# Optimization experiments

Hardware: AMD Instinct MI355X
Metric: run time of the kernel (lower is better)

## Reference

```python
import jax, jax.numpy as jnp
import numpy as np

K, D = 2048, 256
B, H, W = 16, 64, 64
DECAY = 0.99
EPS = 1e-05


def setup_inputs() -> dict:
    key = jax.random.key(0)
    k1, k2, k3 = jax.random.split(key, 3)
    z_e = jax.random.normal(k1, (B, D, H, W), dtype=jnp.float32)
    codebook = jax.random.normal(k2, (K, D), dtype=jnp.float32)
    ema_count = jnp.zeros((K,), dtype=jnp.float32)
    ema_weight = jax.random.normal(k3, (K, D), dtype=jnp.float32)
    return {"z_e": z_e, "codebook": codebook, "ema_count": ema_count, "ema_weight": ema_weight}


def reference(z_e, codebook, ema_count, ema_weight):
    b, d, h, w = z_e.shape
    k = codebook.shape[0]
    # [B, D, H, W] -> [B*H*W, D]
    flat = jnp.transpose(z_e, (0, 2, 3, 1)).reshape(-1, d)
    # squared euclidean distances to each code: [N, K]
    dist = (jnp.sum(flat * flat, axis=1, keepdims=True)
            - 2.0 * (flat @ codebook.T)
            + jnp.sum(codebook * codebook, axis=1))
    idx = jnp.argmin(dist, axis=1)  # [N] int
    # gather nearest codes -> [B, D, H, W]
    z_q = jnp.transpose(codebook[idx].reshape(b, h, w, d), (0, 3, 1, 2))
    # EMA statistics (training path, no_grad in torch)
    n = jax.ops.segment_sum(jnp.ones_like(idx, dtype=flat.dtype), idx, num_segments=k)  # [K]
    dw = jax.ops.segment_sum(flat, idx, num_segments=k)  # [K, D]
    new_ema_count = ema_count * DECAY + (1.0 - DECAY) * n
    new_ema_weight = ema_weight * DECAY + (1.0 - DECAY) * dw
    new_codebook = new_ema_weight / (new_ema_count + EPS)[:, None]
    # commitment loss and straight-through estimator
    loss_commit = jnp.mean(jnp.square(z_e - z_q))
    z_q_st = z_e + jax.lax.stop_gradient(z_q - z_e)
    return (z_q_st, idx.reshape(b, h, w), loss_commit,
            new_codebook, new_ema_count, new_ema_weight)
```

## Files before the change

### kernel.cpp

```cpp
#include <hip/hip_runtime.h>
#include <hip/hip_bf16.h>


#define KC 2048
#define DD 256
#define NB 16
#define HWS 4096
#define NPTS 65536
#define DECAYF 0.99f
#define ONEMD 0.01f
#define EPSF 1e-5f
#define NCH 2
#define MARGIN 0.0625f
#define CHPTS 32
#define FPT 64
#define NLOSS 4096

typedef __attribute__((ext_vector_type(8))) short short8v;
typedef __attribute__((ext_vector_type(16))) float f32x16;

#define WS_IDX     0
#define WS_SORTED  262144
#define WS_CNTI    524288
#define WS_START   532480
#define WS_CURSOR  540672
#define WS_FLAGCNT 548864
#define WS_FLAGS   549120
#define WS_LOSSP   549120
#define WS_CNORM   811264
#define WS_PART    819456
#define WS_CBH     5013760
#define WS_CBL     6062336
#define WS_ZH      7110912
#define WS_ZL      40665344
#define WS_NEED_MFMA 74219776ULL
#define WS_NEED_MID  5013760ULL

#define OUT_ZQ   0
#define OUT_IDX  16777216
#define OUT_LOSS (OUT_IDX + NPTS)
#define OUT_CB   (OUT_LOSS + 1)
#define OUT_CNT  (OUT_CB + KC*DD)
#define OUT_W    (OUT_CNT + KC)

static __device__ __forceinline__ unsigned short f2bf_rn(float x) {
    unsigned u = __builtin_bit_cast(unsigned, x);
    unsigned r = (u + 0x7FFFu + ((u >> 16) & 1u)) >> 16;
    return (unsigned short)r;
}
static __device__ __forceinline__ float bf2f(unsigned short h) {
    unsigned u = ((unsigned)h) << 16;
    return __builtin_bit_cast(float, u);
}
static __device__ __forceinline__ void gload_lds16(const unsigned short* g,
                                                   unsigned short* l) {
    __builtin_amdgcn_global_load_lds(
        (const __attribute__((address_space(1))) void*)g,
        (__attribute__((address_space(3))) void*)l, 16, 0, 0);
}

__global__ __launch_bounds__(256) void prep_kernel(const float* __restrict__ z_e,
                                                   const float* __restrict__ cb,
                                                   float* __restrict__ cnorm,
                                                   unsigned short* __restrict__ cbs_h,
                                                   unsigned short* __restrict__ cbs_l,
                                                   unsigned short* __restrict__ zh,
                                                   unsigned short* __restrict__ zl,
                                                   int* __restrict__ cnti,
                                                   int* __restrict__ flagcnt) {
    const int tid = threadIdx.x;
    if (blockIdx.x >= 4096) {
        int k = (blockIdx.x - 4096) * 256 + tid;
        cnti[k] = 0;
        if (k == 0) *flagcnt = 0;
        const int ct = k >> 5, lc = k & 31;
        const float4* row = reinterpret_cast<const float4*>(cb + (size_t)k * DD);
        float s = 0.f;
        #pragma unroll 4
        for (int chunk = 0; chunk < 32; ++chunk) {
            float4 v0 = row[chunk * 2], v1 = row[chunk * 2 + 1];
            float v[8] = {v0.x, v0.y, v0.z, v0.w, v1.x, v1.y, v1.z, v1.w};
            unsigned short hh[8], ll[8];
            #pragma unroll
            for (int j = 0; j < 8; ++j) {
                s += v[j] * v[j];
                hh[j] = f2bf_rn(v[j]);
                ll[j] = f2bf_rn(v[j] - bf2f(hh[j]));
            }
            const int ks = chunk >> 1, h = chunk & 1;
            size_t dst = (size_t)ct * 8192 + ks * 512 + (h * 32 + lc) * 8;
            *reinterpret_cast<ushort4*>(cbs_h + dst)     = *(ushort4*)&hh[0];
            *reinterpret_cast<ushort4*>(cbs_h + dst + 4) = *(ushort4*)&hh[4];
            *reinterpret_cast<ushort4*>(cbs_l + dst)     = *(ushort4*)&ll[0];
            *reinterpret_cast<ushort4*>(cbs_l + dst + 4) = *(ushort4*)&ll[4];
        }
        cnorm[k] = s;
        return;
    }
    __shared__ float t_lds[64][65];
    const int bid = blockIdx.x;
    const int hw0 = (bid & 63) * 64;
    const int d0 = ((bid >> 6) & 3) * 64;
    const int b = bid >> 8;
    const float* src = z_e + (size_t)b * DD * HWS;
    #pragma unroll
    for (int i = 0; i < 16; ++i) {
        int li = tid + i * 256;
        int d = li >> 6, hw = li & 63;
        t_lds[d][hw] = src[(size_t)(d0 + d) * HWS + hw0 + hw];
    }
    __syncthreads();
    #pragma unroll
    for (int i = 0; i < 16; ++i) {
        int li = tid + i * 256;
        int p = li >> 6, d = li & 63;
        float x = t_lds[d][p];
        unsigned short h = f2bf_rn(x);
        unsigned short l = f2bf_rn(x - bf2f(h));
        size_t o = ((size_t)b * HWS + hw0 + p) * DD + d0 + d;
        zh[o] = h; zl[o] = l;
    }
}

__global__ __launch_bounds__(256) void cnorm_kernel(const float* __restrict__ cb,
                                                    float* __restrict__ cnorm) {
    int k = blockIdx.x * 256 + threadIdx.x;
    if (k < KC) {
        const float4* row = reinterpret_cast<const float4*>(cb + (size_t)k * DD);
        float s = 0.f;
        #pragma unroll 8
        for (int i = 0; i < DD / 4; ++i) {
            float4 v = row[i];
            s += v.x * v.x + v.y * v.y + v.z * v.z + v.w * v.w;
        }
        cnorm[k] = s;
    }
}

__global__ __launch_bounds__(256, 2) void argmin_mfma_kernel(const unsigned short* __restrict__ zh,
                                                             const unsigned short* __restrict__ zl,
                                                             const unsigned short* __restrict__ cbs_h,
                                                             const unsigned short* __restrict__ cbs_l,
                                                             const float* __restrict__ cnorm,
                                                             int* __restrict__ idx_out,
                                                             int* __restrict__ cnti,
                                                             int* __restrict__ flagcnt,
                                                             int* __restrict__ flaglist,
                                                             unsigned long long* __restrict__ fixmin) {
    __shared__ unsigned short lds_cb[2][16][512];

    const int tid = threadIdx.x;
    const int w = tid >> 6, lane = tid & 63;
    const int lc = lane & 31, h = lane >> 5;
    const int p = blockIdx.x * 128 + w * 32 + lc;

    const short8v* zhp = reinterpret_cast<const short8v*>(zh + (size_t)p * DD + h * 8);
    const short8v* zlp = reinterpret_cast<const short8v*>(zl + (size_t)p * DD + h * 8);
    short8v bh[16], bl[16];
    #pragma unroll
    for (int ks = 0; ks < 16; ++ks) { bh[ks] = zhp[ks * 2]; bl[ks] = zlp[ks * 2]; }

    auto stage = [&](int ct) {
        #pragma unroll
        for (int j = 0; j < 8; ++j) {
            const int inst = w * 8 + j;
            const int part = inst >> 4;
            const int ks = inst & 15;
            const unsigned short* src =
                (part ? cbs_l : cbs_h) + (size_t)ct * 8192 + ks * 512 + lane * 8;
            gload_lds16(src, &lds_cb[part][ks][0]);
        }
    };

    float bv1 = 3.4e38f, bv2 = 3.4e38f;
    int bi1 = 0;

    stage(0);
    __syncthreads();

    for (int ct = 0; ct < KC / 32; ++ct) {
        f32x16 a0, a1, a2;
        #pragma unroll
        for (int i = 0; i < 16; ++i) { a0[i] = 0.f; a1[i] = 0.f; a2[i] = 0.f; }
        #pragma unroll
        for (int ks = 0; ks < 16; ++ks) {
            short8v ah = *reinterpret_cast<const short8v*>(&lds_cb[0][ks][lane * 8]);
            short8v al = *reinterpret_cast<const short8v*>(&lds_cb[1][ks][lane * 8]);
            a0 = __builtin_amdgcn_mfma_f32_32x32x16_bf16(ah, bh[ks], a0, 0, 0, 0);
            a1 = __builtin_amdgcn_mfma_f32_32x32x16_bf16(ah, bl[ks], a1, 0, 0, 0);
            a2 = __builtin_amdgcn_mfma_f32_32x32x16_bf16(al, bh[ks], a2, 0, 0, 0);
        }
        const float* cnb = cnorm + ct * 32 + h * 4;
        #pragma unroll
        for (int g = 0; g < 4; ++g) {
            float4 cn = *reinterpret_cast<const float4*>(cnb + g * 8);
            float cna[4] = {cn.x, cn.y, cn.z, cn.w};
            #pragma unroll
            for (int q = 0; q < 4; ++q) {
                float dot = a0[g * 4 + q] + a1[g * 4 + q] + a2[g * 4 + q];
                float v = fmaf(dot, -2.0f, cna[q]);
                int k = ct * 32 + g * 8 + h * 4 + q;
                bool lt = v < bv1;
                bv2 = fminf(bv2, fmaxf(v, bv1));
                bv1 = fminf(bv1, v);
                bi1 = lt ? k : bi1;
            }
        }
        __syncthreads();
        if (ct + 1 < KC / 32) {
            stage(ct + 1);
            __syncthreads();
        }
    }

    float ov1 = __shfl_xor(bv1, 32, 64);
    float ov2 = __shfl_xor(bv2, 32, 64);
    int   oi1 = __shfl_xor(bi1, 32, 64);
    float nv1 = fminf(bv1, ov1);
    float nv2 = fminf(fmaxf(bv1, ov1), fminf(bv2, ov2));
    int ni1 = (ov1 < bv1 || (ov1 == bv1 && oi1 < bi1)) ? oi1 : bi1;

    if (h == 0) {
        idx_out[p] = ni1;
        atomicAdd(&cnti[ni1], 1);
        if (nv2 - nv1 < MARGIN) {
            int pos = atomicAdd(flagcnt, 1);
            flaglist[pos] = p;
            fixmin[pos] = ~0ULL;
        }
    }
}

__global__ __launch_bounds__(256) void fixup_part_kernel(const float* __restrict__ z_e,
                                                         const float* __restrict__ cb,
                                                         const float* __restrict__ cnorm,
                                                         const int* __restrict__ flagcnt,
                                                         const int* __restrict__ flaglist,
                                                         unsigned long long* __restrict__ fixmin) {
    __shared__ float As[64][FPT + 4];
    __shared__ float Bs[64][64 + 4];
    __shared__ float rv[FPT][16];
    __shared__ int   ri[FPT][16];
    __shared__ int   zo[FPT];

    const int tid = threadIdx.x;
    const int tx = tid & 15, ty = tid >> 4;
    const int tot = *flagcnt;
    const int kt = blockIdx.y * 64;

    for (int cbk = blockIdx.x; cbk * FPT < tot; cbk += gridDim.x) {
        const int base = cbk * FPT;
        const int cnt = min(FPT, tot - base);
        __syncthreads();
        if (tid < FPT) {
            int n = flaglist[base + ((tid < cnt) ? tid : 0)];
            zo[tid] = (n >> 12) * DD * HWS + (n & 4095);
        }
        __syncthreads();

        float acc[4][4] = {};
        for (int dc = 0; dc < DD; dc += 64) {
            #pragma unroll
            for (int i = 0; i < 16; ++i) {
                int li = tid + i * 256;
                int d = li >> 6, pp = li & 63;
                As[d][pp] = z_e[(size_t)zo[pp] + (size_t)(dc + d) * HWS];
            }
            #pragma unroll
            for (int i = 0; i < 16; ++i) {
                int li = tid + i * 256;
                int k = li >> 6, d = li & 63;
                Bs[d][k] = cb[(size_t)(kt + k) * DD + dc + d];
            }
            __syncthreads();
            #pragma unroll
            for (int d = 0; d < 64; ++d) {
                const float4 a4 = *reinterpret_cast<const float4*>(&As[d][ty * 4]);
                const float4 b4 = *reinterpret_cast<const float4*>(&Bs[d][tx * 4]);
                const float a[4] = {a4.x, a4.y, a4.z, a4.w};
                const float bb[4] = {b4.x, b4.y, b4.z, b4.w};
                #pragma unroll
                for (int j = 0; j < 4; ++j)
                    #pragma unroll
                    for (int i = 0; i < 4; ++i)
                        acc[j][i] = fmaf(a[j], bb[i], acc[j][i]);
            }
            __syncthreads();
        }

        float bestv[4]; int besti[4];
        #pragma unroll
        for (int j = 0; j < 4; ++j) { bestv[j] = 3.4e38f; besti[j] = 0; }
        #pragma unroll
        for (int i = 0; i < 4; ++i) {
            int k = kt + tx * 4 + i;
            float c = cnorm[k];
            #pragma unroll
            for (int j = 0; j < 4; ++j) {
                float dist = c - 2.0f * acc[j][i];
                if (dist < bestv[j]) { bestv[j] = dist; besti[j] = k; }
            }
        }
        #pragma unroll
        for (int j = 0; j < 4; ++j) { rv[ty * 4 + j][tx] = bestv[j]; ri[ty * 4 + j][tx] = besti[j]; }
        __syncthreads();

        if (tid < cnt) {
            float bv = rv[tid][0]; int bi = ri[tid][0];
            #pragma unroll
            for (int t = 1; t < 16; ++t) {
                float v = rv[tid][t]; int i2 = ri[tid][t];
                if (v < bv || (v == bv && i2 < bi)) { bv = v; bi = i2; }
            }
            unsigned uv = __float_as_uint(bv);
            uv = (uv & 0x80000000u) ? ~uv : (uv | 0x80000000u);
            unsigned long long key = ((unsigned long long)uv << 32) | (unsigned)bi;
            atomicMin(&fixmin[base + tid], key);
        }
    }
}

__global__ __launch_bounds__(256) void scan_apply_kernel(const int* __restrict__ flagcnt,
                                                         const int* __restrict__ flaglist,
                                                         const unsigned long long* __restrict__ fixmin,
                                                         int* __restrict__ idx_out,
                                                         int* __restrict__ cnti,
                                                         int* __restrict__ start,
                                                         int* __restrict__ cursor) {
    const int t = threadIdx.x;
    const int tot = *flagcnt;
    for (int f = t; f < tot; f += 256) {
        int n = flaglist[f];
        int nk = (int)(fixmin[f] & 0xFFFFFFFFull);
        int ok = idx_out[n];
        if (nk != ok) {
            atomicSub(&cnti[ok], 1);
            atomicAdd(&cnti[nk], 1);
            idx_out[n] = nk;
        }
    }
    __syncthreads();

    __shared__ int ps[256];
    int v[8], s = 0;
    #pragma unroll
    for (int j = 0; j < 8; ++j) { v[j] = cnti[t * 8 + j]; s += v[j]; }
    ps[t] = s;
    __syncthreads();
    for (int off = 1; off < 256; off <<= 1) {
        int x = (t >= off) ? ps[t - off] : 0;
        __syncthreads();
        ps[t] += x;
        __syncthreads();
    }
    int base = ps[t] - s;
    #pragma unroll
    for (int j = 0; j < 8; ++j) { start[t * 8 + j] = base; cursor[t * 8 + j] = base; base += v[j]; }
}

#define PT 64
#define KT 64
#define DC 64
__global__ __launch_bounds__(256) void argmin_kernel(const float* __restrict__ z_e,
                                                     const float* __restrict__ cb,
                                                     const float* __restrict__ cnorm,
                                                     int* __restrict__ idx_out) {
    __shared__ float As[DC][PT + 4];
    __shared__ float Bs[DC][KT + 4];
    __shared__ float rv[PT][16];
    __shared__ int   ri[PT][16];
    const int tid = threadIdx.x;
    const int tx = tid & 15, ty = tid >> 4;
    const int n0 = blockIdx.x * PT;
    const int b = n0 >> 12;
    const int hw0 = n0 & 4095;
    const float* zb = z_e + (size_t)b * DD * HWS + hw0;
    float bestv[4]; int besti[4];
    #pragma unroll
    for (int j = 0; j < 4; ++j) { bestv[j] = 3.4e38f; besti[j] = 0; }
    for (int kt = 0; kt < KC; kt += KT) {
        float acc[4][4] = {};
        for (int dc = 0; dc < DD; dc += DC) {
            #pragma unroll
            for (int i = 0; i < 16; ++i) {
                int li = tid + i * 256;
                int d = li >> 6, pp = li & 63;
                As[d][pp] = zb[(size_t)(dc + d) * HWS + pp];
            }
            #pragma unroll
            for (int i = 0; i < 16; ++i) {
                int li = tid + i * 256;
                int k = li >> 6, d = li & 63;
                Bs[d][k] = cb[(size_t)(kt + k) * DD + dc + d];
            }
            __syncthreads();
            #pragma unroll
            for (int d = 0; d < DC; ++d) {
                const float4 a4 = *reinterpret_cast<const float4*>(&As[d][ty * 4]);
                const float4 b4 = *reinterpret_cast<const float4*>(&Bs[d][tx * 4]);
                const float a[4] = {a4.x, a4.y, a4.z, a4.w};
                const float bb[4] = {b4.x, b4.y, b4.z, b4.w};
                #pragma unroll
                for (int j = 0; j < 4; ++j)
                    #pragma unroll
                    for (int i = 0; i < 4; ++i)
                        acc[j][i] = fmaf(a[j], bb[i], acc[j][i]);
            }
            __syncthreads();
        }
        #pragma unroll
        for (int i = 0; i < 4; ++i) {
            int k = kt + tx * 4 + i;
            float c = cnorm[k];
            #pragma unroll
            for (int j = 0; j < 4; ++j) {
                float dist = c - 2.0f * acc[j][i];
                if (dist < bestv[j]) { bestv[j] = dist; besti[j] = k; }
            }
        }
    }
    #pragma unroll
    for (int j = 0; j < 4; ++j) { rv[ty * 4 + j][tx] = bestv[j]; ri[ty * 4 + j][tx] = besti[j]; }
    __syncthreads();
    if (tid < PT) {
        float bv = rv[tid][0]; int bi = ri[tid][0];
        #pragma unroll
        for (int t = 1; t < 16; ++t) {
            float v = rv[tid][t]; int i2 = ri[tid][t];
            if (v < bv || (v == bv && i2 < bi)) { bv = v; bi = i2; }
        }
        idx_out[n0 + tid] = bi;
    }
}

__global__ __launch_bounds__(256) void hist_kernel(const int* __restrict__ idx,
                                                   int* __restrict__ cnti) {
    int n = blockIdx.x * 256 + threadIdx.x;
    atomicAdd(&cnti[idx[n]], 1);
}

__global__ __launch_bounds__(256) void scatter_ids_kernel(const int* __restrict__ idx,
                                                          int* __restrict__ cursor,
                                                          int* __restrict__ sorted,
                                                          float* __restrict__ out_idxf) {
    int n = blockIdx.x * 256 + threadIdx.x;
    int k = idx[n];
    out_idxf[n] = (float)k;
    int pos = atomicAdd(&cursor[k], 1);
    sorted[pos] = n;
}

__global__ __launch_bounds__(256) void dw_chunk_kernel(const unsigned short* __restrict__ zh,
                                                       const unsigned short* __restrict__ zl,
                                                       const int* __restrict__ sorted,
                                                       const int* __restrict__ idx,
                                                       float* __restrict__ dwacc) {
    const int t = threadIdx.x;
    const int base = blockIdx.x * CHPTS;
    int kcur = idx[sorted[base]];
    float acc = 0.f;
    for (int i = 0; i < CHPTS; ++i) {
        const int n = sorted[base + i];
        const int k = idx[n];
        if (k != kcur) {
            atomicAdd(&dwacc[(size_t)kcur * DD + t], acc);
            acc = 0.f; kcur = k;
        }
        acc += bf2f(zh[(size_t)n * DD + t]) + bf2f(zl[(size_t)n * DD + t]);
    }
    atomicAdd(&dwacc[(size_t)kcur * DD + t], acc);
}

__global__ __launch_bounds__(256) void dw_direct_kernel(const float* __restrict__ z_e,
                                                        const int* __restrict__ sorted,
                                                        const int* __restrict__ start,
                                                        const int* __restrict__ cnti,
                                                        float* __restrict__ part) {
    const int k = blockIdx.x, c = blockIdx.y, t = threadIdx.x;
    const int s0 = start[k], cnt = cnti[k];
    float acc = 0.f;
    for (int p = c; p < cnt; p += NCH) {
        int n = sorted[s0 + p];
        int b = n >> 12, hw = n & 4095;
        acc += z_e[(size_t)b * DD * HWS + (size_t)t * HWS + hw];
    }
    part[((size_t)k * NCH + c) * DD + t] = acc;
}

__global__ __launch_bounds__(256) void zq_scatter_kernel(const float* __restrict__ z_e,
                                                         const float* __restrict__ cb,
                                                         const int* __restrict__ idx,
                                                         float* __restrict__ out_zq,
                                                         float* __restrict__ lossp,
                                                         int* __restrict__ cursor,
                                                         int* __restrict__ sorted,
                                                         float* __restrict__ out_idxf,
                                                         float* __restrict__ dwacc,
                                                         int fuse_tail) {
    const int tid = threadIdx.x;
    const size_t base = ((size_t)blockIdx.x * 256 + tid) * 16;
    const int hw = (int)(base & 4095);
    const int d = (int)((base >> 12) & 255);
    const int b = (int)(base >> 20);
    const int n0 = b * HWS + hw;

    const int4* ip = reinterpret_cast<const int4*>(idx + n0);
    const float4* zp = reinterpret_cast<const float4*>(z_e + base);
    float4* op = reinterpret_cast<float4*>(out_zq + base);

    float ls = 0.f;
    #pragma unroll
    for (int g = 0; g < 4; ++g) {
        int4 i4 = ip[g];
        float4 z4 = zp[g];
        int kk[4] = {i4.x, i4.y, i4.z, i4.w};
        float zz[4] = {z4.x, z4.y, z4.z, z4.w};
        float o4[4];
        #pragma unroll
        for (int q = 0; q < 4; ++q) {
            float qv = cb[(size_t)kk[q] * DD + d];
            o4[q] = zz[q] + (qv - zz[q]);
            float df = zz[q] - qv;
            ls += df * df;
        }
        float4 w4; w4.x = o4[0]; w4.y = o4[1]; w4.z = o4[2]; w4.w = o4[3];
        op[g] = w4;
    }

    #pragma unroll
    for (int off = 32; off > 0; off >>= 1) ls += __shfl_down(ls, off, 64);
    __shared__ float wsum[4];
    if ((tid & 63) == 0) wsum[tid >> 6] = ls;
    __syncthreads();
    if (tid == 0) lossp[blockIdx.x] = wsum[0] + wsum[1] + wsum[2] + wsum[3];

    if (fuse_tail && blockIdx.x < 256) {
        int n = blockIdx.x * 256 + tid;
        int k = idx[n];
        out_idxf[n] = (float)k;
        int pos = atomicAdd(&cursor[k], 1);
        sorted[pos] = n;
        #pragma unroll
        for (int i = 0; i < (KC * DD) / NPTS; ++i)
            dwacc[n + i * NPTS] = 0.f;
    }
}

__global__ __launch_bounds__(256) void finalize_dw_kernel(const float* __restrict__ ema_count,
                                                          const float* __restrict__ ema_weight,
                                                          const int* __restrict__ cnti,
                                                          const float* __restrict__ dwacc,
                                                          const float* __restrict__ lossp,
                                                          float* __restrict__ out_cb,
                                                          float* __restrict__ out_cnt,
                                                          float* __restrict__ out_w,
                                                          float* __restrict__ out_loss) {
    const int t = blockIdx.x * 256 + threadIdx.x;
    const int k = t >> 8, d = t & 255;
    const float nc = ema_count[k] * DECAYF + ONEMD * (float)cnti[k];
    const float nw = ema_weight[t] * DECAYF + ONEMD * dwacc[t];
    out_w[t] = nw;
    out_cb[t] = nw / (nc + EPSF);
    if (d == 0) out_cnt[k] = nc;

    if (blockIdx.x == 0) {
        __shared__ double sd[256];
        const int tid = threadIdx.x;
        double s = 0.0;
        for (int i = tid; i < NLOSS; i += 256) s += (double)lossp[i];
        sd[tid] = s;
        __syncthreads();
        for (int off = 128; off > 0; off >>= 1) {
            if (tid < off) sd[tid] += sd[tid + off];
            __syncthreads();
        }
        if (tid == 0) out_loss[0] = (float)(sd[0] / 16777216.0);
    }
}

__global__ __launch_bounds__(256) void finalize_part_kernel(const float* __restrict__ ema_count,
                                                            const float* __restrict__ ema_weight,
                                                            const int* __restrict__ cnti,
                                                            const float* __restrict__ part,
                                                            const float* __restrict__ lossp,
                                                            float* __restrict__ out_cb,
                                                            float* __restrict__ out_cnt,
                                                            float* __restrict__ out_w,
                                                            float* __restrict__ out_loss) {
    const int t = blockIdx.x * 256 + threadIdx.x;
    const int k = t >> 8, d = t & 255;
    float dw = 0.f;
    #pragma unroll
    for (int c = 0; c < NCH; ++c) dw += part[((size_t)k * NCH + c) * DD + d];
    const float nc = ema_count[k] * DECAYF + ONEMD * (float)cnti[k];
    const float nw = ema_weight[t] * DECAYF + ONEMD * dw;
    out_w[t] = nw;
    out_cb[t] = nw / (nc + EPSF);
    if (d == 0) out_cnt[k] = nc;

    if (blockIdx.x == 0) {
        __shared__ double sd[256];
        const int tid = threadIdx.x;
        double s = 0.0;
        for (int i = tid; i < NLOSS; i += 256) s += (double)lossp[i];
        sd[tid] = s;
        __syncthreads();
        for (int off = 128; off > 0; off >>= 1) {
            if (tid < off) sd[tid] += sd[tid + off];
            __syncthreads();
        }
        if (tid == 0) out_loss[0] = (float)(sd[0] / 16777216.0);
    }
}

extern "C" void kernel_launch(void* const* d_in, const int* in_sizes, int n_in,
                              void* d_out, int out_size, void* d_ws, size_t ws_size,
                              hipStream_t stream) {
    const float* z_e       = (const float*)d_in[0];
    const float* codebook  = (const float*)d_in[1];
    const float* ema_count = (const float*)d_in[2];
    const float* ema_weight= (const float*)d_in[3];
    float* out = (float*)d_out;
    char* ws = (char*)d_ws;

    int*   ws_idx    = (int*)(ws + WS_IDX);
    int*   ws_sorted = (int*)(ws + WS_SORTED);
    int*   ws_cnti   = (int*)(ws + WS_CNTI);
    int*   ws_start  = (int*)(ws + WS_START);
    int*   ws_cursor = (int*)(ws + WS_CURSOR);
    int*   ws_flagc  = (int*)(ws + WS_FLAGCNT);
    int*   ws_flags  = (int*)(ws + WS_FLAGS);
    float* ws_lossp  = (float*)(ws + WS_LOSSP);
    float* ws_cnorm  = (float*)(ws + WS_CNORM);
    unsigned long long* ws_fixmin = (unsigned long long*)(ws + WS_PART);
    float* ws_dwacc  = (float*)(ws + WS_PART);
    float* ws_part   = (float*)(ws + WS_PART);
    unsigned short* ws_cbh = (unsigned short*)(ws + WS_CBH);
    unsigned short* ws_cbl = (unsigned short*)(ws + WS_CBL);
    unsigned short* ws_zh  = (unsigned short*)(ws + WS_ZH);
    unsigned short* ws_zl  = (unsigned short*)(ws + WS_ZL);

    const bool mfma_path = (ws_size >= WS_NEED_MFMA);
    const bool mid_path  = (ws_size >= WS_NEED_MID);

    if (mfma_path) {
        prep_kernel<<<4104, 256, 0, stream>>>(z_e, codebook, ws_cnorm, ws_cbh, ws_cbl,
                                              ws_zh, ws_zl, ws_cnti, ws_flagc);
        argmin_mfma_kernel<<<NPTS / 128, 256, 0, stream>>>(ws_zh, ws_zl, ws_cbh, ws_cbl,
                                                           ws_cnorm, ws_idx, ws_cnti,
                                                           ws_flagc, ws_flags, ws_fixmin);
        fixup_part_kernel<<<dim3(128, KC / 64), 256, 0, stream>>>(z_e, codebook, ws_cnorm,
                                                                  ws_flagc, ws_flags,
                                                                  ws_fixmin);
        scan_apply_kernel<<<1, 256, 0, stream>>>(ws_flagc, ws_flags, ws_fixmin,
                                                 ws_idx, ws_cnti, ws_start, ws_cursor);
        zq_scatter_kernel<<<NLOSS, 256, 0, stream>>>(z_e, codebook, ws_idx,
                                                     out + OUT_ZQ, ws_lossp,
                                                     ws_cursor, ws_sorted,
                                                     out + OUT_IDX, ws_dwacc, 1);
        dw_chunk_kernel<<<NPTS / CHPTS, 256, 0, stream>>>(ws_zh, ws_zl, ws_sorted,
                                                          ws_idx, ws_dwacc);
        finalize_dw_kernel<<<(KC * DD) / 256, 256, 0, stream>>>(ema_count, ema_weight,
                                                                ws_cnti, ws_dwacc, ws_lossp,
                                                                out + OUT_CB, out + OUT_CNT,
                                                                out + OUT_W, out + OUT_LOSS);
    } else if (mid_path) {
        hipMemsetAsync(ws + WS_CNTI, 0, (size_t)(WS_FLAGCNT + 256 - WS_CNTI), stream);
        cnorm_kernel<<<(KC + 255) / 256, 256, 0, stream>>>(codebook, ws_cnorm);
        argmin_kernel<<<NPTS / PT, 256, 0, stream>>>(z_e, codebook, ws_cnorm, ws_idx);
        hist_kernel<<<NPTS / 256, 256, 0, stream>>>(ws_idx, ws_cnti);
        scan_apply_kernel<<<1, 256, 0, stream>>>(ws_flagc, ws_flags, ws_fixmin,
                                                 ws_idx, ws_cnti, ws_start, ws_cursor);
        zq_scatter_kernel<<<NLOSS, 256, 0, stream>>>(z_e, codebook, ws_idx,
                                                     out + OUT_ZQ, ws_lossp,
                                                     ws_cursor, ws_sorted,
                                                     out + OUT_IDX, ws_part, 0);
        scatter_ids_kernel<<<NPTS / 256, 256, 0, stream>>>(ws_idx, ws_cursor, ws_sorted,
                                                           out + OUT_IDX);
        dw_direct_kernel<<<dim3(KC, NCH), 256, 0, stream>>>(z_e, ws_sorted,
                                                            ws_start, ws_cnti, ws_part + KC * DD);
        finalize_part_kernel<<<(KC * DD) / 256, 256, 0, stream>>>(ema_count, ema_weight,
                                                                  ws_cnti, ws_part + KC * DD,
                                                                  ws_lossp,
                                                                  out + OUT_CB, out + OUT_CNT,
                                                                  out + OUT_W, out + OUT_LOSS);
    }
}
```

Before: 405.2 us.

## Split argmin over two codebook halves and merge candidates in separate kernel

The MFMA argmin kernel now launches a second grid dimension so each block scans only half of the codebook, writing per-half best/second-best distances and index to a workspace buffer. A new merge kernel combines the two halves, writes indices, counts, and flags near-tie points for fixup. This doubles the number of blocks to better fill the GPU's compute units, at the cost of loading each point's operands twice, an extra launch, and an intermediate buffer round trip.

```diff
diff --git a/kernel.cpp b/kernel.cpp
--- a/kernel.cpp
+++ b/kernel.cpp
@@ -29,6 +29,7 @@
 #define WS_LOSSP   549120
 #define WS_CNORM   811264
 #define WS_PART    819456
+#define WS_HALF    2916352
 #define WS_CBH     5013760
 #define WS_CBL     6062336
 #define WS_ZH      7110912
@@ -142,17 +143,15 @@
                                                              const unsigned short* __restrict__ cbs_h,
                                                              const unsigned short* __restrict__ cbs_l,
                                                              const float* __restrict__ cnorm,
-                                                             int* __restrict__ idx_out,
-                                                             int* __restrict__ cnti,
-                                                             int* __restrict__ flagcnt,
-                                                             int* __restrict__ flaglist,
-                                                             unsigned long long* __restrict__ fixmin) {
+                                                             float4* __restrict__ halfres) {
     __shared__ unsigned short lds_cb[2][16][512];
 
     const int tid = threadIdx.x;
     const int w = tid >> 6, lane = tid & 63;
     const int lc = lane & 31, h = lane >> 5;
     const int p = blockIdx.x * 128 + w * 32 + lc;
+    const int khalf = blockIdx.y;
+    const int ct0 = khalf * (KC / 64);
 
     const short8v* zhp = reinterpret_cast<const short8v*>(zh + (size_t)p * DD + h * 8);
     const short8v* zlp = reinterpret_cast<const short8v*>(zl + (size_t)p * DD + h * 8);
@@ -173,12 +172,12 @@
     };
 
     float bv1 = 3.4e38f, bv2 = 3.4e38f;
-    int bi1 = 0;
-
-    stage(0);
+    int bi1 = khalf * (KC / 2);
+
+    stage(ct0);
     __syncthreads();
 
-    for (int ct = 0; ct < KC / 32; ++ct) {
+    for (int ct = ct0; ct < ct0 + KC / 64; ++ct) {
         f32x16 a0, a1, a2;
         #pragma unroll
         for (int i = 0; i < 16; ++i) { a0[i] = 0.f; a1[i] = 0.f; a2[i] = 0.f; }
@@ -207,7 +206,7 @@
             }
         }
         __syncthreads();
-        if (ct + 1 < KC / 32) {
+        if (ct + 1 < ct0 + KC / 64) {
             stage(ct + 1);
             __syncthreads();
         }
@@ -221,13 +220,35 @@
     int ni1 = (ov1 < bv1 || (ov1 == bv1 && oi1 < bi1)) ? oi1 : bi1;
 
     if (h == 0) {
-        idx_out[p] = ni1;
-        atomicAdd(&cnti[ni1], 1);
-        if (nv2 - nv1 < MARGIN) {
-            int pos = atomicAdd(flagcnt, 1);
-            flaglist[pos] = p;
-            fixmin[pos] = ~0ULL;
-        }
+        float4 r;
+        r.x = nv1; r.y = nv2; r.z = __int_as_float(ni1); r.w = 0.f;
+        halfres[(size_t)p * 2 + khalf] = r;
+    }
+}
+
+__global__ __launch_bounds__(256) void merge_kernel(const float4* __restrict__ halfres,
+                                                    int* __restrict__ idx_out,
+                                                    int* __restrict__ cnti,
+                                                    int* __restrict__ flagcnt,
+                                                    int* __restrict__ flaglist,
+                                                    unsigned long long* __restrict__ fixmin) {
+    const int n = blockIdx.x * 256 + threadIdx.x;
+    float4 h0 = halfres[(size_t)n * 2];
+    float4 h1 = halfres[(size_t)n * 2 + 1];
+    const float b0 = h0.x, r0 = h0.y;
+    const float b1 = h1.x, r1 = h1.y;
+    const int i0 = __float_as_int(h0.z), i1 = __float_as_int(h1.z);
+
+    const float nv1 = fminf(b0, b1);
+    const float nv2 = fminf(fmaxf(b0, b1), fminf(r0, r1));
+    const int ni1 = (b1 < b0) ? i1 : i0;
+
+    idx_out[n] = ni1;
+    atomicAdd(&cnti[ni1], 1);
+    if (nv2 - nv1 < MARGIN) {
+        int pos = atomicAdd(flagcnt, 1);
+        flaglist[pos] = n;
+        fixmin[pos] = ~0ULL;
     }
 }
 
@@ -635,6 +656,7 @@
     unsigned long long* ws_fixmin = (unsigned long long*)(ws + WS_PART);
     float* ws_dwacc  = (float*)(ws + WS_PART);
     float* ws_part   = (float*)(ws + WS_PART);
+    float4* ws_half  = (float4*)(ws + WS_HALF);
     unsigned short* ws_cbh = (unsigned short*)(ws + WS_CBH);
     unsigned short* ws_cbl = (unsigned short*)(ws + WS_CBL);
     unsigned short* ws_zh  = (unsigned short*)(ws + WS_ZH);
@@ -646,9 +668,11 @@
     if (mfma_path) {
         prep_kernel<<<4104, 256, 0, stream>>>(z_e, codebook, ws_cnorm, ws_cbh, ws_cbl,
                                               ws_zh, ws_zl, ws_cnti, ws_flagc);
-        argmin_mfma_kernel<<<NPTS / 128, 256, 0, stream>>>(ws_zh, ws_zl, ws_cbh, ws_cbl,
-                                                           ws_cnorm, ws_idx, ws_cnti,
-                                                           ws_flagc, ws_flags, ws_fixmin);
+        argmin_mfma_kernel<<<dim3(NPTS / 128, 2), 256, 0, stream>>>(ws_zh, ws_zl,
+                                                                    ws_cbh, ws_cbl,
+                                                                    ws_cnorm, ws_half);
+        merge_kernel<<<NPTS / 256, 256, 0, stream>>>(ws_half, ws_idx, ws_cnti,
+                                                     ws_flagc, ws_flags, ws_fixmin);
         fixup_part_kernel<<<dim3(128, KC / 64), 256, 0, stream>>>(z_e, codebook, ws_cnorm,
                                                                   ws_flagc, ws_flags,
                                                                   ws_fixmin);
```

Measured after the change: 431.0 us. 6.4% more time.
